# Optimization experiments

Hardware: AMD Instinct MI355X
Metric: run time of the kernel (lower is better)

The kernel has to match this reference:

```python
import jax, jax.numpy as jnp
import numpy as np

D_MODEL, D_K, D_V, N_HEADS = 1024, 64, 64, 16
B, S = 2, 2048
LN_EPS = 1e-5


def setup_inputs() -> dict:
    key = jax.random.key(0)
    ks = jax.random.split(key, 12)
    s = 1.0 / np.sqrt(D_MODEL)
    inp = {
        "Q": jax.random.normal(ks[0], (B, S, D_MODEL), jnp.float32),
        "K": jax.random.normal(ks[1], (B, S, D_MODEL), jnp.float32),
        "V": jax.random.normal(ks[2], (B, S, D_MODEL), jnp.float32),
        "attn_mask": jax.random.bernoulli(ks[3], 0.1, (B, S, S)),
        "Wq": jax.random.uniform(ks[4], (D_MODEL, D_K * N_HEADS), jnp.float32, -s, s),
        "bq": jnp.zeros((D_K * N_HEADS,), jnp.float32),
        "Wk": jax.random.uniform(ks[5], (D_MODEL, D_K * N_HEADS), jnp.float32, -s, s),
        "bk": jnp.zeros((D_K * N_HEADS,), jnp.float32),
        "Wv": jax.random.uniform(ks[6], (D_MODEL, D_V * N_HEADS), jnp.float32, -s, s),
        "bv": jnp.zeros((D_V * N_HEADS,), jnp.float32),
        "Wo": jax.random.uniform(ks[7], (N_HEADS * D_V, D_MODEL), jnp.float32, -s, s),
        "bo": jnp.zeros((D_MODEL,), jnp.float32),
        "gamma": jnp.ones((D_MODEL,), jnp.float32),
        "beta": jnp.zeros((D_MODEL,), jnp.float32),
    }
    return inp


def reference(Q, K, V, attn_mask, Wq, bq, Wk, bk, Wv, bv, Wo, bo, gamma, beta):
    b, s, _ = Q.shape
    # projections -> [B, S, H, d]
    q = (Q @ Wq + bq).reshape(b, s, N_HEADS, D_K)
    k = (K @ Wk + bk).reshape(b, -1, N_HEADS, D_K)
    v = (V @ Wv + bv).reshape(b, -1, N_HEADS, D_V)
    # scores [B, H, Sq, Sk]
    scores = jnp.einsum("bqhd,bkhd->bhqk", q, k) / np.sqrt(D_K).astype(np.float32)
    scores = jnp.where(attn_mask[:, None, :, :], jnp.float32(-1e9), scores)
    attn = jax.nn.softmax(scores, axis=-1)
    context = jnp.einsum("bhqk,bkhd->bqhd", attn, v).reshape(b, s, N_HEADS * D_V)
    out = context @ Wo + bo + Q  # residual
    mu = jnp.mean(out, axis=-1, keepdims=True)
    var = jnp.var(out, axis=-1, keepdims=True)
    return (out - mu) * jax.lax.rsqrt(var + LN_EPS) * gamma + beta
```

## Files before the change

### kernel.cpp

```cpp
#include <hip/hip_runtime.h>
#include <hip/hip_bf16.h>
#include <math.h>


#define D_MODEL 1024
#define NHEADS  16
#define DHEAD   64
#define BATCH   2
#define SEQ     2048
#define MROWS   (BATCH * SEQ)
#define SCLF    0.18033688f

typedef __attribute__((ext_vector_type(8)))  short bf16x8;
typedef __attribute__((ext_vector_type(4)))  float f32x4;
typedef __attribute__((ext_vector_type(16))) float f32x16;

__device__ inline unsigned short f2bf(float f) {
    unsigned int u = __builtin_bit_cast(unsigned int, f);
    unsigned int r = (u + 0x7FFFu + ((u >> 16) & 1u)) >> 16;
    return (unsigned short)r;
}

__device__ inline unsigned cvtpk_bf16(float lo, float hi2) {
    unsigned r;
    asm("v_cvt_pk_bf16_f32 %0, %1, %2" : "=v"(r) : "v"(lo), "v"(hi2));
    return r;
}

__device__ inline void gload16(const unsigned short* g, unsigned short* lbase, int lane) {
#if __has_builtin(__builtin_amdgcn_global_load_lds)
    __builtin_amdgcn_global_load_lds(
        (const __attribute__((address_space(1))) unsigned int*)g,
        (__attribute__((address_space(3))) unsigned int*)lbase, 16, 0, 0);
#else
    *(bf16x8*)(lbase + lane * 8) = *(const bf16x8*)g;
#endif
}

__global__ __launch_bounds__(256) void detect_mask_par(
    const unsigned int* __restrict__ m, int nwords, int* __restrict__ flags)
{
    const int i = blockIdx.x * 256 + threadIdx.x;
    int a = 0, b = 0;
    if (i < nwords) {
        const unsigned int w = m[i];
        a = (w != 0u && w != 1u);
        b = (w != 0u && w != 0x3F800000u);
    }
    const int wa = (int)__any(a);
    const int wb = (int)__any(b);
    if ((threadIdx.x & 63) == 0) {
        if (wa) atomicOr(&flags[0], 1);
        if (wb) atomicOr(&flags[1], 1);
    }
}

__global__ __launch_bounds__(256) void cvt_all(
    const float* __restrict__ Q, const float* __restrict__ K,
    const float* __restrict__ V,
    const float* __restrict__ w0, const float* __restrict__ w1,
    const float* __restrict__ w2, const float* __restrict__ w3,
    unsigned short* __restrict__ Qb, unsigned short* __restrict__ Kb,
    unsigned short* __restrict__ Vb,
    unsigned short* __restrict__ t0, unsigned short* __restrict__ t1,
    unsigned short* __restrict__ t2, unsigned short* __restrict__ t3,
    const void* __restrict__ mask, const int* __restrict__ flags,
    unsigned long long* __restrict__ mbits, int nwords)
{
    __shared__ float tile[64][65];
    const int z = blockIdx.z;
    if (z < 3) {
        const float* s = (z == 0) ? Q : (z == 1) ? K : V;
        unsigned short* d = (z == 0) ? Qb : (z == 1) ? Kb : Vb;
        const int i = blockIdx.x * 256 + threadIdx.x;
        float4 a = ((const float4*)s)[i * 2];
        float4 b = ((const float4*)s)[i * 2 + 1];
        unsigned u0 = cvtpk_bf16(a.x, a.y);
        unsigned u1 = cvtpk_bf16(a.z, a.w);
        unsigned u2 = cvtpk_bf16(b.x, b.y);
        unsigned u3 = cvtpk_bf16(b.z, b.w);
        ((int4*)d)[i] = make_int4((int)u0, (int)u1, (int)u2, (int)u3);
    } else if (z < 7) {
        if (blockIdx.x >= 256) return;
        const int wz = z - 3;
        const float* W = (wz == 0) ? w0 : (wz == 1) ? w1 : (wz == 2) ? w2 : w3;
        unsigned short* T = (wz == 0) ? t0 : (wz == 1) ? t1 : (wz == 2) ? t2 : t3;
        const int n0 = (blockIdx.x & 15) * 64;
        const int k0 = (blockIdx.x >> 4) * 64;
        const int t  = threadIdx.x;
        const int r  = t >> 4;
        const int c4 = (t & 15) * 4;
        #pragma unroll
        for (int u = 0; u < 4; ++u) {
            float4 v = *(const float4*)(W + (size_t)(k0 + r + u * 16) * D_MODEL + n0 + c4);
            tile[r + u * 16][c4 + 0] = v.x;
            tile[r + u * 16][c4 + 1] = v.y;
            tile[r + u * 16][c4 + 2] = v.z;
            tile[r + u * 16][c4 + 3] = v.w;
        }
        __syncthreads();
        #pragma unroll
        for (int u = 0; u < 4; ++u) {
            const int nr = r + u * 16;
            ushort4 o;
            o.x = f2bf(tile[c4 + 0][nr]);
            o.y = f2bf(tile[c4 + 1][nr]);
            o.z = f2bf(tile[c4 + 2][nr]);
            o.w = f2bf(tile[c4 + 3][nr]);
            *(ushort4*)(T + (size_t)(n0 + nr) * D_MODEL + k0 + c4) = o;
        }
    } else {
        const int lane   = threadIdx.x & 63;
        const int wv     = blockIdx.x * 4 + (threadIdx.x >> 6);
        const int nwaves = gridDim.x * 4;
        const int mf = (flags[0] == 0) ? 0 : (flags[1] == 0) ? 1 : 2;
        for (int w = wv; w < nwords; w += nwaves) {
            bool bit;
            if (mf == 0)      bit = ((const unsigned int*)mask)[(size_t)w * 64 + lane] != 0u;
            else if (mf == 1) bit = ((const float*)mask)[(size_t)w * 64 + lane] != 0.f;
            else              bit = ((const unsigned char*)mask)[(size_t)w * 64 + lane] != 0;
            const unsigned long long bb = __ballot(bit);
            if (lane == 0) mbits[w] = bb;
        }
    }
}

#define BKQ 32
__global__ __launch_bounds__(256, 1) void gemm_qkv(
    const unsigned short* __restrict__ A0, const unsigned short* __restrict__ A1,
    const unsigned short* __restrict__ A2,
    const unsigned short* __restrict__ B0, const unsigned short* __restrict__ B1,
    const unsigned short* __restrict__ B2,
    const float* __restrict__ bias0, const float* __restrict__ bias1,
    const float* __restrict__ bias2,
    unsigned short* __restrict__ C0, unsigned short* __restrict__ C1,
    unsigned short* __restrict__ C2)
{
    const int z = blockIdx.z;
    const unsigned short* A  = (z == 0) ? A0 : (z == 1) ? A1 : A2;
    const unsigned short* Bt = (z == 0) ? B0 : (z == 1) ? B1 : B2;
    const float* bias        = (z == 0) ? bias0 : (z == 1) ? bias1 : bias2;
    unsigned short* C        = (z == 0) ? C0 : (z == 1) ? C1 : C2;
    const int K = D_MODEL, N = D_MODEL;

    __shared__ unsigned short As[2][128 * BKQ];
    __shared__ unsigned short Bs[2][128 * BKQ];
    const int tid  = threadIdx.x;
    const int w    = tid >> 6;
    const int lane = tid & 63;
    const int lo   = lane & 15;
    const int hi   = lane >> 4;
    const int wm   = (w >> 1) * 64;
    const int wn   = (w & 1) * 64;
    const int m0   = blockIdx.x * 128;
    const int n0   = blockIdx.y * 128;

    const unsigned short* Ab = A  + (size_t)m0 * K;
    const unsigned short* Bb = Bt + (size_t)n0 * K;

    f32x4 acc[4][4];
    #pragma unroll
    for (int i = 0; i < 4; ++i)
        #pragma unroll
        for (int j = 0; j < 4; ++j) acc[i][j] = (f32x4){0.f, 0.f, 0.f, 0.f};

    const int NT = K / BKQ;
    auto stage = [&](int buf, int t) {
        const int k0 = t * BKQ;
        #pragma unroll
        for (int i = 0; i < 2; ++i) {
            const int c = i * 256 + tid;
            gload16(Ab + (size_t)(c >> 2) * K + k0 + (c & 3) * 8,
                    &As[buf][(i * 256 + w * 64) * 8], lane);
        }
        #pragma unroll
        for (int i = 0; i < 2; ++i) {
            const int c = i * 256 + tid;
            gload16(Bb + (size_t)(c >> 2) * K + k0 + (c & 3) * 8,
                    &Bs[buf][(i * 256 + w * 64) * 8], lane);
        }
    };

    stage(0, 0);
    __syncthreads();
    int cur = 0;
    for (int t = 0; t < NT; ++t) {
        if (t + 1 < NT) stage(cur ^ 1, t + 1);
        bf16x8 af[4], bfr[4];
        #pragma unroll
        for (int f = 0; f < 4; ++f) {
            af[f]  = *(const bf16x8*)&As[cur][(wm + f * 16 + lo) * BKQ + hi * 8];
            bfr[f] = *(const bf16x8*)&Bs[cur][(wn + f * 16 + lo) * BKQ + hi * 8];
        }
        #pragma unroll
        for (int fm = 0; fm < 4; ++fm)
            #pragma unroll
            for (int fn = 0; fn < 4; ++fn)
                acc[fm][fn] = __builtin_amdgcn_mfma_f32_16x16x32_bf16(
                    af[fm], bfr[fn], acc[fm][fn], 0, 0, 0);
        __syncthreads();
        cur ^= 1;
    }

    #pragma unroll
    for (int fm = 0; fm < 4; ++fm) {
        const int row = m0 + wm + fm * 16 + hi * 4;
        #pragma unroll
        for (int fn = 0; fn < 4; ++fn) {
            const int col = n0 + wn + fn * 16 + lo;
            const float bv = bias[col];
            #pragma unroll
            for (int r = 0; r < 4; ++r) {
                float o = acc[fm][fn][r] + bv;
                if (z == 0) o *= SCLF;
                if (z < 2)
                    C[(size_t)(row + r) * N + col] = f2bf(o);
                else
                    C[(size_t)((row + r) >> 11) * 2097152
                      + (size_t)col * 2048 + ((row + r) & 2047)] = f2bf(o);
            }
        }
    }
}

__global__ __launch_bounds__(256) void gemm_out32(
    const unsigned short* __restrict__ A, const unsigned short* __restrict__ Bt,
    const float* __restrict__ bias, const float* __restrict__ resid,
    float* __restrict__ C)
{
    const int K = D_MODEL, N = D_MODEL;
    __shared__ unsigned short As[2][64 * 32];
    __shared__ unsigned short Bs[2][64 * 32];
    const int tid  = threadIdx.x;
    const int w    = tid >> 6;
    const int lane = tid & 63;
    const int lo   = lane & 15;
    const int hi   = lane >> 4;
    const int wm   = (w >> 1) * 32;
    const int wn   = (w & 1) * 32;
    const int m0   = blockIdx.x * 64;
    const int n0   = blockIdx.y * 64;

    const unsigned short* Ab = A  + (size_t)m0 * K;
    const unsigned short* Bb = Bt + (size_t)n0 * K;

    f32x4 acc[2][2];
    #pragma unroll
    for (int i = 0; i < 2; ++i)
        #pragma unroll
        for (int j = 0; j < 2; ++j) acc[i][j] = (f32x4){0.f, 0.f, 0.f, 0.f};

    const int NT = K / 32;
    auto stage = [&](int buf, int t) {
        const int k0 = t * 32;
        gload16(Ab + (size_t)(tid >> 2) * K + k0 + (tid & 3) * 8,
                &As[buf][(w * 64) * 8], lane);
        gload16(Bb + (size_t)(tid >> 2) * K + k0 + (tid & 3) * 8,
                &Bs[buf][(w * 64) * 8], lane);
    };

    stage(0, 0);
    __syncthreads();
    int cur = 0;
    for (int t = 0; t < NT; ++t) {
        if (t + 1 < NT) stage(cur ^ 1, t + 1);
        bf16x8 af[2], bfr[2];
        #pragma unroll
        for (int f = 0; f < 2; ++f) {
            af[f]  = *(const bf16x8*)&As[cur][(wm + f * 16 + lo) * 32 + hi * 8];
            bfr[f] = *(const bf16x8*)&Bs[cur][(wn + f * 16 + lo) * 32 + hi * 8];
        }
        #pragma unroll
        for (int fm = 0; fm < 2; ++fm)
            #pragma unroll
            for (int fn = 0; fn < 2; ++fn)
                acc[fm][fn] = __builtin_amdgcn_mfma_f32_16x16x32_bf16(
                    af[fm], bfr[fn], acc[fm][fn], 0, 0, 0);
        __syncthreads();
        cur ^= 1;
    }

    #pragma unroll
    for (int fm = 0; fm < 2; ++fm) {
        const int row = m0 + wm + fm * 16 + hi * 4;
        #pragma unroll
        for (int fn = 0; fn < 2; ++fn) {
            const int col = n0 + wn + fn * 16 + lo;
            const float bv = bias[col];
            #pragma unroll
            for (int r = 0; r < 4; ++r)
                C[(size_t)(row + r) * N + col] =
                    acc[fm][fn][r] + bv + resid[(size_t)(row + r) * N + col];
        }
    }
}

__global__ __launch_bounds__(512, 2) void attn_mfma32(
    const unsigned short* __restrict__ qb, const unsigned short* __restrict__ kbm,
    const unsigned short* __restrict__ vt,
    const unsigned long long* __restrict__ mbits, unsigned short* __restrict__ ctx)
{
    __shared__ __align__(16) unsigned char smem[34304];
    const int tid  = threadIdx.x;
    const int w8   = tid >> 6;
    const int g    = w8 >> 2;
    const int wq   = w8 & 3;
    const int lane = tid & 63;
    const int l31  = lane & 31;
    const int hi   = lane >> 5;
    const int h    = blockIdx.x;
    const int q0   = blockIdx.y * 128;
    const int b    = blockIdx.z;

    unsigned short* KsG = (unsigned short*)smem + (size_t)g * 4096;
    unsigned short* VsG = (unsigned short*)(smem + 16384) + (size_t)g * 4096;

    const size_t qkbase = (size_t)b * SEQ * D_MODEL + (size_t)h * DHEAD;
    const size_t vtbase = ((size_t)b * D_MODEL + h * DHEAD) * SEQ;

    const int qtok = q0 + wq * 32 + l31;
    bf16x8 qA[4];
    #pragma unroll
    for (int s = 0; s < 4; ++s)
        qA[s] = *(const bf16x8*)(qb + qkbase + (size_t)qtok * D_MODEL + s * 16 + hi * 8);

    const int4 ones_i = make_int4(0x3F803F80, 0x3F803F80, 0x3F803F80, 0x3F803F80);
    const bf16x8 ones = __builtin_bit_cast(bf16x8, ones_i);

    f32x16 o0 = {}, o1 = {}, accl = {};

    const unsigned long long* mrow = mbits + ((size_t)b * SEQ + qtok) * (SEQ / 64);

    const int krow = wq * 8 + (lane >> 3);
    const int kc   = lane & 7;
    const int kswz = kc ^ (krow & 7);
    const int vrow = wq * 16 + (lane >> 2);
    const int vsrc = ((lane & 3) - (vrow >> 1)) & 3;

    const unsigned short* kl = kbm + qkbase + (size_t)(g * 1024 + krow) * D_MODEL + kswz * 8;
    const unsigned short* vl = vt + vtbase + (size_t)vrow * SEQ + g * 1024 + vsrc * 8;
    const int kldb = (wq * 8) * 64;
    const int vldb = (wq * 16) * 32;

    auto stage = [&](int buf) {
        gload16(kl, &KsG[buf * 2048 + kldb], lane);
        gload16(vl, &VsG[buf * 2048 + vldb], lane);
        kl += (size_t)32 * D_MODEL;
        vl += 32;
    };

    stage(0);
    unsigned long long mw64 = mrow[g * 16];
    __syncthreads();
    int cur = 0;

    for (int t = 0; t < 32; ++t) {
        if (t + 1 < 32) stage(cur ^ 1);
        const unsigned int mw = (unsigned int)(mw64 >> (32 * (t & 1) + 4 * hi));
        if ((t & 1) && t + 1 < 32) mw64 = mrow[g * 16 + ((t + 1) >> 1)];

        f32x16 st = {};
        __builtin_amdgcn_s_setprio(1);
        #pragma unroll
        for (int s = 0; s < 4; ++s) {
            bf16x8 kf = *(const bf16x8*)&KsG[cur * 2048 + l31 * 64 + ((2 * s + hi) ^ (l31 & 7)) * 8];
            st = __builtin_amdgcn_mfma_f32_32x32x16_bf16(kf, qA[s], st, 0, 0, 0);
        }
        __builtin_amdgcn_s_setprio(0);

        #pragma unroll
        for (int r = 0; r < 16; ++r) {
            const int klo = (r & 3) + 8 * (r >> 2);
            const float x = ((mw >> klo) & 1u) ? -1e9f : st[r];
            st[r] = exp2f(x);
        }

        bf16x8 pa[2];
        #pragma unroll
        for (int s = 0; s < 2; ++s) {
            const int base = s * 8;
            unsigned av  = cvtpk_bf16(st[base + 0], st[base + 1]);
            unsigned bv2 = cvtpk_bf16(st[base + 4], st[base + 5]);
            unsigned cv  = cvtpk_bf16(st[base + 2], st[base + 3]);
            unsigned dv  = cvtpk_bf16(st[base + 6], st[base + 7]);
            asm("v_permlane32_swap_b32 %0, %1" : "+v"(av), "+v"(bv2));
            asm("v_permlane32_swap_b32 %0, %1" : "+v"(cv), "+v"(dv));
            int4 pk = make_int4((int)av, (int)cv, (int)bv2, (int)dv);
            pa[s] = __builtin_bit_cast(bf16x8, pk);
        }

        __builtin_amdgcn_s_setprio(1);
        #pragma unroll
        for (int s = 0; s < 2; ++s) {
            const int slot = ((2 * s + hi) + (l31 >> 1)) & 3;
            bf16x8 vf0 = *(const bf16x8*)&VsG[cur * 2048 + l31 * 32 + slot * 8];
            o0 = __builtin_amdgcn_mfma_f32_32x32x16_bf16(pa[s], vf0, o0, 0, 0, 0);
            bf16x8 vf1 = *(const bf16x8*)&VsG[cur * 2048 + (32 + l31) * 32 + slot * 8];
            o1 = __builtin_amdgcn_mfma_f32_32x32x16_bf16(pa[s], vf1, o1, 0, 0, 0);
            accl = __builtin_amdgcn_mfma_f32_32x32x16_bf16(pa[s], ones, accl, 0, 0, 0);
        }
        __builtin_amdgcn_s_setprio(0);
        __syncthreads();
        cur ^= 1;
    }

    __syncthreads();
    float* comb  = (float*)smem;
    float* lvals = (float*)(smem + 33792);
    if (g == 1) {
        float* p = comb + (size_t)(wq * 64 + lane) * 33;
        #pragma unroll
        for (int r = 0; r < 16; ++r) { p[r] = o0[r]; p[16 + r] = o1[r]; }
        if (l31 == 0) {
            #pragma unroll
            for (int r = 0; r < 16; ++r)
                lvals[wq * 32 + (r & 3) + 8 * (r >> 2) + 4 * hi] = accl[r];
        }
    }
    __syncthreads();
    if (g == 0) {
        const float* p = comb + (size_t)(wq * 64 + lane) * 33;
        #pragma unroll
        for (int r = 0; r < 16; ++r) {
            const int qloc = (r & 3) + 8 * (r >> 2) + 4 * hi;
            const float inv = 1.f / (accl[r] + lvals[wq * 32 + qloc]);
            unsigned short* dst = ctx + qkbase + (size_t)(q0 + wq * 32 + qloc) * D_MODEL;
            dst[l31]      = f2bf((o0[r] + p[r]) * inv);
            dst[32 + l31] = f2bf((o1[r] + p[16 + r]) * inv);
        }
    }
}

__global__ __launch_bounds__(256) void layernorm1024(
    const float* __restrict__ x, const float* __restrict__ gamma,
    const float* __restrict__ beta, float* __restrict__ out)
{
    const int row = blockIdx.x;
    const int tid = threadIdx.x;
    const float* xr = x + (size_t)row * D_MODEL;
    float4 v = *(const float4*)(xr + (tid << 2));
    float s = v.x + v.y + v.z + v.w;
    float q = v.x * v.x + v.y * v.y + v.z * v.z + v.w * v.w;
    #pragma unroll
    for (int off = 1; off < 64; off <<= 1) {
        s += __shfl_xor(s, off, 64);
        q += __shfl_xor(q, off, 64);
    }
    __shared__ float sw[4], qw_[4];
    const int wid = tid >> 6;
    if ((tid & 63) == 0) { sw[wid] = s; qw_[wid] = q; }
    __syncthreads();
    s = sw[0] + sw[1] + sw[2] + sw[3];
    q = qw_[0] + qw_[1] + qw_[2] + qw_[3];
    const float mu  = s * (1.f / D_MODEL);
    const float var = q * (1.f / D_MODEL) - mu * mu;
    const float a = var + 1e-5f;
    float inv = rsqrtf(a);
    inv = inv * (1.5f - 0.5f * a * inv * inv);
    float4 gg = *(const float4*)(gamma + (tid << 2));
    float4 bt = *(const float4*)(beta + (tid << 2));
    float4 o;
    o.x = (v.x - mu) * inv * gg.x + bt.x;
    o.y = (v.y - mu) * inv * gg.y + bt.y;
    o.z = (v.z - mu) * inv * gg.z + bt.z;
    o.w = (v.w - mu) * inv * gg.w + bt.w;
    *(float4*)(out + (size_t)row * D_MODEL + (tid << 2)) = o;
}

extern "C" void kernel_launch(void* const* d_in, const int* in_sizes, int n_in,
                              void* d_out, int out_size, void* d_ws, size_t ws_size,
                              hipStream_t stream)
{
    const float* Q    = (const float*)d_in[0];
    const float* K    = (const float*)d_in[1];
    const float* V    = (const float*)d_in[2];
    const void*  mask = d_in[3];
    const float* Wq   = (const float*)d_in[4];
    const float* bq   = (const float*)d_in[5];
    const float* Wk   = (const float*)d_in[6];
    const float* bk   = (const float*)d_in[7];
    const float* Wv   = (const float*)d_in[8];
    const float* bv   = (const float*)d_in[9];
    const float* Wo   = (const float*)d_in[10];
    const float* bo   = (const float*)d_in[11];
    const float* gam  = (const float*)d_in[12];
    const float* bet  = (const float*)d_in[13];
    float* out = (float*)d_out;

    const size_t NE = (size_t)MROWS * D_MODEL;
    const size_t WE = (size_t)D_MODEL * D_MODEL;
    const size_t NMW = (size_t)BATCH * SEQ * (SEQ / 64);
    unsigned short* Qbf = (unsigned short*)d_ws;
    unsigned short* Kbf = Qbf + NE;
    unsigned short* Vbf = Kbf + NE;
    unsigned short* qb  = Vbf + NE;
    unsigned short* kb  = qb + NE;
    unsigned short* vt  = kb + NE;
    unsigned short* Wt0 = vt + NE;
    unsigned short* Wt1 = Wt0 + WE;
    unsigned short* Wt2 = Wt1 + WE;
    unsigned short* Wt3 = Wt2 + WE;
    unsigned long long* mbits = (unsigned long long*)(Wt3 + WE);
    int* mflags = (int*)(mbits + NMW);
    unsigned short* ctxb = Qbf;
    float* outp = (float*)Kbf;
    if (ws_size < 6 * NE * 2 + 4 * WE * 2 + NMW * 8 + 64) return;

    hipMemsetAsync(mflags, 0, 2 * sizeof(int), stream);
    detect_mask_par<<<256, 256, 0, stream>>>((const unsigned int*)mask, 65536, mflags);

    cvt_all<<<dim3(2048, 1, 8), 256, 0, stream>>>(Q, K, V, Wq, Wk, Wv, Wo,
                                                  Qbf, Kbf, Vbf, Wt0, Wt1, Wt2, Wt3,
                                                  mask, mflags, mbits, (int)NMW);

    gemm_qkv<<<dim3(32, 8, 3), 256, 0, stream>>>(Qbf, Kbf, Vbf, Wt0, Wt1, Wt2,
                                                 bq, bk, bv, qb, kb, vt);

    dim3 ag(NHEADS, SEQ / 128, BATCH);
    attn_mfma32<<<ag, 512, 0, stream>>>(qb, kb, vt, mbits, ctxb);

    gemm_out32<<<dim3(64, 16), 256, 0, stream>>>(ctxb, Wt3, bo, Q, outp);

    layernorm1024<<<MROWS, 256, 0, stream>>>(outp, gam, bet, out);
}
```

Before: 180.1 us.

## Software-pipeline attention loop: overlap QK^T of next tile with PV of previous

Restructures the attention main loop into a software pipeline. Each iteration now computes QK^T for the current K tile and issues the PV MFMAs for the previous tile's probabilities in the same block, followed by a prologue and an epilogue. It moves from double to triple buffering of K/V in LDS (smem grows from about 34KB to 48KB) so staging, score MFMAs and PV MFMAs can overlap. The aim is to hide the exp/convert latency behind matrix work. The cost is more LDS per block, which may reduce occupancy at 2 blocks per CU, and extra registers for the carried probabilities.

```diff
diff --git a/kernel.cpp b/kernel.cpp
--- a/kernel.cpp
+++ b/kernel.cpp
@@ -300,7 +300,7 @@
     const unsigned short* __restrict__ vt,
     const unsigned long long* __restrict__ mbits, unsigned short* __restrict__ ctx)
 {
-    __shared__ __align__(16) unsigned char smem[34304];
+    __shared__ __align__(16) unsigned char smem[49152];
     const int tid  = threadIdx.x;
     const int w8   = tid >> 6;
     const int g    = w8 >> 2;
@@ -312,8 +312,8 @@
     const int q0   = blockIdx.y * 128;
     const int b    = blockIdx.z;
 
-    unsigned short* KsG = (unsigned short*)smem + (size_t)g * 4096;
-    unsigned short* VsG = (unsigned short*)(smem + 16384) + (size_t)g * 4096;
+    unsigned short* KsG = (unsigned short*)(smem + (size_t)g * 12288);
+    unsigned short* VsG = (unsigned short*)(smem + 24576 + (size_t)g * 12288);
 
     const size_t qkbase = (size_t)b * SEQ * D_MODEL + (size_t)h * DHEAD;
     const size_t vtbase = ((size_t)b * D_MODEL + h * DHEAD) * SEQ;
@@ -349,33 +349,29 @@
         vl += 32;
     };
 
+    bf16x8 paP[2];
+    unsigned long long mw64 = mrow[g * 16];
+
     stage(0);
-    unsigned long long mw64 = mrow[g * 16];
-    __syncthreads();
-    int cur = 0;
-
-    for (int t = 0; t < 32; ++t) {
-        if (t + 1 < 32) stage(cur ^ 1);
-        const unsigned int mw = (unsigned int)(mw64 >> (32 * (t & 1) + 4 * hi));
-        if ((t & 1) && t + 1 < 32) mw64 = mrow[g * 16 + ((t + 1) >> 1)];
-
+    __syncthreads();
+    stage(1);
+
+    {
+        const unsigned int mw = (unsigned int)(mw64 >> (4 * hi));
         f32x16 st = {};
         __builtin_amdgcn_s_setprio(1);
         #pragma unroll
         for (int s = 0; s < 4; ++s) {
-            bf16x8 kf = *(const bf16x8*)&KsG[cur * 2048 + l31 * 64 + ((2 * s + hi) ^ (l31 & 7)) * 8];
+            bf16x8 kf = *(const bf16x8*)&KsG[0 * 2048 + l31 * 64 + ((2 * s + hi) ^ (l31 & 7)) * 8];
             st = __builtin_amdgcn_mfma_f32_32x32x16_bf16(kf, qA[s], st, 0, 0, 0);
         }
         __builtin_amdgcn_s_setprio(0);
-
         #pragma unroll
         for (int r = 0; r < 16; ++r) {
             const int klo = (r & 3) + 8 * (r >> 2);
             const float x = ((mw >> klo) & 1u) ? -1e9f : st[r];
             st[r] = exp2f(x);
         }
-
-        bf16x8 pa[2];
         #pragma unroll
         for (int s = 0; s < 2; ++s) {
             const int base = s * 8;
@@ -386,23 +382,68 @@
             asm("v_permlane32_swap_b32 %0, %1" : "+v"(av), "+v"(bv2));
             asm("v_permlane32_swap_b32 %0, %1" : "+v"(cv), "+v"(dv));
             int4 pk = make_int4((int)av, (int)cv, (int)bv2, (int)dv);
-            pa[s] = __builtin_bit_cast(bf16x8, pk);
-        }
-
+            paP[s] = __builtin_bit_cast(bf16x8, pk);
+        }
+    }
+    __syncthreads();
+
+    int bp = 0, bc = 1, bn = 2;
+    for (int t = 1; t < 32; ++t) {
+        if (t + 1 < 32) stage(bn);
+        const unsigned int mw = (unsigned int)(mw64 >> (32 * (t & 1) + 4 * hi));
+        if ((t & 1) && t + 1 < 32) mw64 = mrow[g * 16 + ((t + 1) >> 1)];
+
+        f32x16 st = {};
         __builtin_amdgcn_s_setprio(1);
+        #pragma unroll
+        for (int s = 0; s < 4; ++s) {
+            bf16x8 kf = *(const bf16x8*)&KsG[bc * 2048 + l31 * 64 + ((2 * s + hi) ^ (l31 & 7)) * 8];
+            st = __builtin_amdgcn_mfma_f32_32x32x16_bf16(kf, qA[s], st, 0, 0, 0);
+        }
         #pragma unroll
         for (int s = 0; s < 2; ++s) {
             const int slot = ((2 * s + hi) + (l31 >> 1)) & 3;
-            bf16x8 vf0 = *(const bf16x8*)&VsG[cur * 2048 + l31 * 32 + slot * 8];
-            o0 = __builtin_amdgcn_mfma_f32_32x32x16_bf16(pa[s], vf0, o0, 0, 0, 0);
-            bf16x8 vf1 = *(const bf16x8*)&VsG[cur * 2048 + (32 + l31) * 32 + slot * 8];
-            o1 = __builtin_amdgcn_mfma_f32_32x32x16_bf16(pa[s], vf1, o1, 0, 0, 0);
-            accl = __builtin_amdgcn_mfma_f32_32x32x16_bf16(pa[s], ones, accl, 0, 0, 0);
+            bf16x8 vf0 = *(const bf16x8*)&VsG[bp * 2048 + l31 * 32 + slot * 8];
+            o0 = __builtin_amdgcn_mfma_f32_32x32x16_bf16(paP[s], vf0, o0, 0, 0, 0);
+            bf16x8 vf1 = *(const bf16x8*)&VsG[bp * 2048 + (32 + l31) * 32 + slot * 8];
+            o1 = __builtin_amdgcn_mfma_f32_32x32x16_bf16(paP[s], vf1, o1, 0, 0, 0);
+            accl = __builtin_amdgcn_mfma_f32_32x32x16_bf16(paP[s], ones, accl, 0, 0, 0);
         }
         __builtin_amdgcn_s_setprio(0);
+
+        #pragma unroll
+        for (int r = 0; r < 16; ++r) {
+            const int klo = (r & 3) + 8 * (r >> 2);
+            const float x = ((mw >> klo) & 1u) ? -1e9f : st[r];
+            st[r] = exp2f(x);
+        }
+        #pragma unroll
+        for (int s = 0; s < 2; ++s) {
+            const int base = s * 8;
+            unsigned av  = cvtpk_bf16(st[base + 0], st[base + 1]);
+            unsigned bv2 = cvtpk_bf16(st[base + 4], st[base + 5]);
+            unsigned cv  = cvtpk_bf16(st[base + 2], st[base + 3]);
+            unsigned dv  = cvtpk_bf16(st[base + 6], st[base + 7]);
+            asm("v_permlane32_swap_b32 %0, %1" : "+v"(av), "+v"(bv2));
+            asm("v_permlane32_swap_b32 %0, %1" : "+v"(cv), "+v"(dv));
+            int4 pk = make_int4((int)av, (int)cv, (int)bv2, (int)dv);
+            paP[s] = __builtin_bit_cast(bf16x8, pk);
+        }
         __syncthreads();
-        cur ^= 1;
-    }
+        const int tmp = bp; bp = bc; bc = bn; bn = tmp;
+    }
+
+    __builtin_amdgcn_s_setprio(1);
+    #pragma unroll
+    for (int s = 0; s < 2; ++s) {
+        const int slot = ((2 * s + hi) + (l31 >> 1)) & 3;
+        bf16x8 vf0 = *(const bf16x8*)&VsG[bp * 2048 + l31 * 32 + slot * 8];
+        o0 = __builtin_amdgcn_mfma_f32_32x32x16_bf16(paP[s], vf0, o0, 0, 0, 0);
+        bf16x8 vf1 = *(const bf16x8*)&VsG[bp * 2048 + (32 + l31) * 32 + slot * 8];
+        o1 = __builtin_amdgcn_mfma_f32_32x32x16_bf16(paP[s], vf1, o1, 0, 0, 0);
+        accl = __builtin_amdgcn_mfma_f32_32x32x16_bf16(paP[s], ones, accl, 0, 0, 0);
+    }
+    __builtin_amdgcn_s_setprio(0);
 
     __syncthreads();
     float* comb  = (float*)smem;
```

New measurement: 196.0 us. 1.09x slower.
